# Kernel optimization log

Measured on AMD Instinct MI355X. Metric: run time of the kernel, lower is better.

Reference implementation:

```python
import jax, jax.numpy as jnp
import numpy as np

D_MODEL = 2048
N_HEADS = 32
N_KVHEADS = 8
HEAD_DIM = D_MODEL // N_HEADS  # 64
N_GROUPS = N_HEADS // N_KVHEADS  # 4
B, L = 2, 2048


def setup_inputs() -> dict:
    key = jax.random.key(0)
    k1, k2, k3 = jax.random.split(key, 3)
    x = jax.random.normal(k1, (B, L, D_MODEL), dtype=jnp.float32)
    W_qkv = jax.random.normal(k2, (D_MODEL, HEAD_DIM * (N_HEADS + 2 * N_KVHEADS)), dtype=jnp.float32) * 0.02
    W_out = jax.random.normal(k3, (D_MODEL, D_MODEL), dtype=jnp.float32) * 0.02
    # additive causal mask, broadcasts over (b, g, h, l, j)
    neg = jnp.float32(-1e9)
    mask = jnp.where(jnp.tril(jnp.ones((L, L), dtype=bool)), jnp.float32(0.0), neg)
    return {"x": x, "mask": mask, "W_qkv": W_qkv, "W_out": W_out}


def reference(x, mask, W_qkv, W_out):
    b, l, _ = x.shape
    qkv = x @ W_qkv  # (b, l, hd*(H + 2*KVH))
    q, k, v = jnp.split(qkv, [N_HEADS * HEAD_DIM, (N_HEADS + N_KVHEADS) * HEAD_DIM], axis=-1)
    # NOTE: faithful to the original: plain row-major reshapes (no seq/head transpose)
    q = q.reshape(b, N_GROUPS, N_KVHEADS, l, HEAD_DIM)  # (b, g, h, l, d)
    k = k.reshape(b, N_KVHEADS, l, HEAD_DIM)            # (b, h, j, d)
    v = v.reshape(b, N_KVHEADS, l, HEAD_DIM)            # (b, h, j, d)
    scores = jnp.einsum('bghld,bhjd->bghlj', q, k) * (HEAD_DIM ** -0.5)
    scores = scores + mask  # mask broadcasts over leading dims
    attn = jax.nn.softmax(scores, axis=-1)
    out = jnp.einsum('bghlj,bhjd->bghld', attn, v)  # (b, g, h, l, d)
    # rearrange 'b g h l d -> b l (g h d)'
    out = jnp.transpose(out, (0, 3, 1, 2, 4)).reshape(b, l, D_MODEL)
    return out @ W_out
```

## Files before the change

### kernel.cpp

```cpp
#include <hip/hip_runtime.h>
#include <stdint.h>


typedef unsigned short u16;
typedef unsigned int u32;
typedef __attribute__((ext_vector_type(8))) short bf16x8;
typedef __attribute__((ext_vector_type(4))) float f32x4;

__device__ __forceinline__ u16 f2bf(float f) {
  union { float f; uint32_t u; } v; v.f = f;
  uint32_t u = v.u;
  u += 0x7fffu + ((u >> 16) & 1u);
  return (u16)(u >> 16);
}

__device__ __forceinline__ f32x4 mfma16(bf16x8 a, bf16x8 b, f32x4 c) {
  return __builtin_amdgcn_mfma_f32_16x16x32_bf16(a, b, c, 0, 0, 0);
}

__device__ __forceinline__ uint32_t cvt_pk_bf16(float a, float b) {
  uint32_t r;
  asm("v_cvt_pk_bf16_f32 %0, %1, %2" : "=v"(r) : "v"(a), "v"(b));
  return r;
}

__device__ __forceinline__ float fmax3(float a, float b, float c) {
  float d;
  asm("v_max3_f32 %0, %1, %2, %3" : "=v"(d) : "v"(a), "v"(b), "v"(c));
  return d;
}

__device__ __forceinline__ float exp2fast(float x) {
  return __builtin_amdgcn_exp2f(x);
}

__device__ __forceinline__ void gload16(const u16* g, u16* l) {
  __builtin_amdgcn_global_load_lds((__attribute__((address_space(1))) void*)g,
                                   (__attribute__((address_space(3))) void*)l, 16, 0, 0);
}

__global__ __launch_bounds__(256) void cvt_f32_bf16(const float* __restrict__ in,
                                                    u16* __restrict__ out, int n4) {
  int i = blockIdx.x * blockDim.x + threadIdx.x;
  if (i < n4) {
    float4 v = ((const float4*)in)[i];
    uint2 o;
    o.x = (uint32_t)f2bf(v.x) | ((uint32_t)f2bf(v.y) << 16);
    o.y = (uint32_t)f2bf(v.z) | ((uint32_t)f2bf(v.w) << 16);
    ((uint2*)out)[i] = o;
  }
}

__global__ __launch_bounds__(256) void transpose_cvt(const float* __restrict__ in,
                                                     u16* __restrict__ out, int R, int C) {
  __shared__ float tile[32][33];
  int c0 = blockIdx.x * 32, r0 = blockIdx.y * 32;
  int tx = threadIdx.x, ty = threadIdx.y;
#pragma unroll
  for (int k = 0; k < 32; k += 8)
    tile[ty + k][tx] = in[(size_t)(r0 + ty + k) * C + c0 + tx];
  __syncthreads();
#pragma unroll
  for (int k = 0; k < 32; k += 8)
    out[(size_t)(c0 + ty + k) * R + r0 + tx] = f2bf(tile[tx][ty + k]);
}

template <bool OUTF32>
__global__ __launch_bounds__(256) void gemm_bf16(const u16* __restrict__ A,
                                                 const u16* __restrict__ Bt,
                                                 void* __restrict__ C,
                                                 int M, int N, int K) {
  __shared__ __align__(16) u16 As[2][128 * 32];
  __shared__ __align__(16) u16 Bs[2][128 * 32];
  int tid = threadIdx.x;
  int lane = tid & 63, w = tid >> 6;
  int wm = (w >> 1) * 64, wn = (w & 1) * 64;

  int nwg = gridDim.x * gridDim.y;
  int lin = blockIdx.y * gridDim.x + blockIdx.x;
  int lin2 = (lin & 7) * (nwg >> 3) + (lin >> 3);
  int bxs = lin2 % gridDim.x, bys = lin2 / gridDim.x;
  int bm = bys * 128, bn = bxs * 128;

  int c = lane & 15, g = lane >> 4;

  const int srow = w * 16 + (lane >> 2);
  const int scol = (((lane & 3) ^ ((lane >> 3) & 3))) * 8;
  const u16* aP = A + (size_t)(bm + srow) * K + scol;
  const u16* bP = Bt + (size_t)(bn + srow) * K + scol;
  const size_t rowskip = (size_t)64 * K;

  f32x4 zero = {0.f, 0.f, 0.f, 0.f};
  f32x4 acc[4][4];
#pragma unroll
  for (int mi = 0; mi < 4; mi++)
#pragma unroll
    for (int ni = 0; ni < 4; ni++) acc[mi][ni] = zero;

  auto STAGE = [&](int kt, int buf) {
    u16* aL = &As[buf][(w * 16) * 32];
    u16* bL = &Bs[buf][(w * 16) * 32];
    gload16(aP + kt, aL);
    gload16(aP + kt + rowskip, aL + 64 * 32);
    gload16(bP + kt, bL);
    gload16(bP + kt + rowskip, bL + 64 * 32);
  };

  const int nk = K >> 5;
  STAGE(0, 0);
  __syncthreads();

  const int fq = (g ^ ((c >> 1) & 3)) * 8;

  for (int t = 0; t < nk; ++t) {
    const int cur = t & 1;
    if (t + 1 < nk) STAGE((t + 1) << 5, cur ^ 1);
    bf16x8 af[4], bfr[4];
#pragma unroll
    for (int i = 0; i < 4; i++) af[i] = *(const bf16x8*)&As[cur][(wm + i * 16 + c) * 32 + fq];
#pragma unroll
    for (int i = 0; i < 4; i++) bfr[i] = *(const bf16x8*)&Bs[cur][(wn + i * 16 + c) * 32 + fq];
#pragma unroll
    for (int mi = 0; mi < 4; mi++)
#pragma unroll
      for (int ni = 0; ni < 4; ni++)
        acc[mi][ni] = mfma16(af[mi], bfr[ni], acc[mi][ni]);
    __syncthreads();
  }

#pragma unroll
  for (int mi = 0; mi < 4; mi++)
#pragma unroll
    for (int ni = 0; ni < 4; ni++)
#pragma unroll
      for (int i = 0; i < 4; i++) {
        int row = bm + wm + mi * 16 + g * 4 + i;
        int col = bn + wn + ni * 16 + c;
        float v = acc[mi][ni][i];
        if (OUTF32)
          ((float*)C)[(size_t)row * N + col] = v;
        else
          ((u16*)C)[(size_t)row * N + col] = f2bf(v);
      }
}

__global__ __launch_bounds__(256, 2) void attn_fwd(const u16* __restrict__ qkv,
                                                   u16* __restrict__ attn) {
  __shared__ __align__(16) u16 Ks[2][64][72];
  __shared__ __align__(16) u16 Vs[2][64][72];
  __shared__ __align__(16) u16 Ps[4][32][64];
  const int tid = threadIdx.x;
  const int lane = tid & 63, w = tid >> 6;
  const int c = lane & 15, g = lane >> 4;
  const float C2 = 0.18033688011112042f;

  const int bid = blockIdx.x;
  const int slot = bid >> 3;
  const int head = (bid & 7) * 8 + (slot >> 3);
  const int p = slot & 7;
  const int qtA = p, qtB = 15 - p;
  const int b = head >> 5, gh = head & 31, h = gh & 7;
  const u16* qb = qkv + (size_t)b * 6291456;
  const int qbaseA = qtA * 128 + w * 32;
  const int qbaseB = qtB * 128 + w * 32;

  const u16* qrowA = qb + (size_t)(gh * 64 + qtA * 4 + w) * 3072;
  const u16* qrowB = qb + (size_t)(gh * 64 + qtB * 4 + w) * 3072;
  bf16x8 qfA[2][2], qfB[2][2];
#pragma unroll
  for (int qs = 0; qs < 2; qs++)
#pragma unroll
    for (int kd = 0; kd < 2; kd++) {
      qfA[qs][kd] = *(const bf16x8*)(qrowA + (qs * 16 + c) * 64 + kd * 32 + g * 8);
      qfB[qs][kd] = *(const bf16x8*)(qrowB + (qs * 16 + c) * 64 + kd * 32 + g * 8);
    }

  const f32x4 zero = {0.f, 0.f, 0.f, 0.f};
  f32x4 oA[2][4], oB[2][4];
#pragma unroll
  for (int qs = 0; qs < 2; qs++)
#pragma unroll
    for (int dt = 0; dt < 4; dt++) { oA[qs][dt] = zero; oB[qs][dt] = zero; }
  float mA[2] = {-1e30f, -1e30f}, sA[2] = {0.f, 0.f};
  float mB[2] = {-1e30f, -1e30f}, sB[2] = {0.f, 0.f};

  const int kj = tid >> 2, kd16 = (tid & 3) * 16;
  const int vj0 = (tid >> 4) * 4, vd = (tid & 15) * 4;
  const int vsw = (tid & 7) << 3;
  uint4 kreg0, kreg1;
  uint2 vreg[4];

  auto LOAD = [&](int t) {
    int j = t * 64 + kj;
    const u16* kr = qb + (size_t)(h * 256 + (j >> 3)) * 3072 + 2048 + (j & 7) * 64;
    kreg0 = *(const uint4*)(kr + kd16);
    kreg1 = *(const uint4*)(kr + kd16 + 8);
#pragma unroll
    for (int r = 0; r < 4; r++) {
      int jv = t * 64 + vj0 + r;
      const u16* vr = qb + (size_t)(h * 256 + (jv >> 3)) * 3072 + 2560 + (jv & 7) * 64;
      vreg[r] = *(const uint2*)(vr + vd);
    }
  };
  auto EX = [](uint2 v, int e) -> uint32_t {
    uint32_t x = (e < 2) ? v.x : v.y;
    return (e & 1) ? (x >> 16) : (x & 0xffffu);
  };
  auto STORE = [&](int buf) {
    *(uint4*)&Ks[buf][kj][kd16] = kreg0;
    *(uint4*)&Ks[buf][kj][kd16 + 8] = kreg1;
#pragma unroll
    for (int e = 0; e < 4; e++) {
      uint2 wv;
      wv.x = EX(vreg[0], e) | (EX(vreg[1], e) << 16);
      wv.y = EX(vreg[2], e) | (EX(vreg[3], e) << 16);
      *(uint2*)&Vs[buf][vd + e][vj0 ^ vsw] = wv;
    }
  };

  auto computeQ = [&](int t, int qbase, bf16x8 (&qf)[2][2], bf16x8 (&kf)[4][2],
                      f32x4 (&o)[2][4], float (&m_i)[2], float (&s_i)[2], int cur) {
    const bool diag = (t * 64 + 63 > qbase);
#pragma unroll
    for (int qs = 0; qs < 2; qs++) {
      f32x4 sc[4];
      __builtin_amdgcn_s_setprio(1);
#pragma unroll
      for (int kvt = 0; kvt < 4; kvt++) {
        f32x4 s = mfma16(kf[kvt][0], qf[qs][0], zero);
        sc[kvt] = mfma16(kf[kvt][1], qf[qs][1], s);
      }
      __builtin_amdgcn_s_setprio(0);
      const int q = qbase + qs * 16 + c;
      if (diag) {
#pragma unroll
        for (int kvt = 0; kvt < 4; kvt++)
#pragma unroll
          for (int i = 0; i < 4; i++)
            if (t * 64 + kvt * 16 + g * 4 + i > q) sc[kvt][i] = -1e30f;
      }
      float tmax = fmax3(sc[0][0], sc[0][1], sc[0][2]);
      tmax = fmax3(tmax, sc[0][3], sc[1][0]);
      tmax = fmax3(tmax, sc[1][1], sc[1][2]);
      tmax = fmax3(tmax, sc[1][3], sc[2][0]);
      tmax = fmax3(tmax, sc[2][1], sc[2][2]);
      tmax = fmax3(tmax, sc[2][3], sc[3][0]);
      tmax = fmax3(tmax, sc[3][1], sc[3][2]);
      tmax = fmaxf(tmax, sc[3][3]);
      tmax = fmaxf(tmax, __shfl_xor(tmax, 16));
      tmax = fmaxf(tmax, __shfl_xor(tmax, 32));
      if (!__all(tmax <= m_i[qs] + 64.0f)) {
        float mn = fmaxf(m_i[qs], tmax);
        float corr = exp2fast((m_i[qs] - mn) * C2);
        m_i[qs] = mn;
        s_i[qs] *= corr;
#pragma unroll
        for (int i = 0; i < 4; i++) {
          float cb = __shfl(corr, g * 4 + i);
#pragma unroll
          for (int dt = 0; dt < 4; dt++) o[qs][dt][i] *= cb;
        }
      }
      const float nmc = -m_i[qs] * C2;
      float rs = 0.f;
#pragma unroll
      for (int kvt = 0; kvt < 4; kvt++)
#pragma unroll
        for (int i = 0; i < 4; i++) {
          float pv = exp2fast(fmaf(sc[kvt][i], C2, nmc));
          sc[kvt][i] = pv;
          rs += pv;
        }
      rs += __shfl_xor(rs, 16);
      rs += __shfl_xor(rs, 32);
      s_i[qs] += rs;
      const int pr = qs * 16 + c;
      const int sw = (c & 7) << 3;
#pragma unroll
      for (int kvt = 0; kvt < 4; kvt++) {
        uint2 pw;
        pw.x = cvt_pk_bf16(sc[kvt][0], sc[kvt][1]);
        pw.y = cvt_pk_bf16(sc[kvt][2], sc[kvt][3]);
        *(uint2*)&Ps[w][pr][(kvt * 16 + g * 4) ^ sw] = pw;
      }
    }
    __builtin_amdgcn_s_setprio(1);
#pragma unroll
    for (int kt2 = 0; kt2 < 2; kt2++) {
      bf16x8 bv[4];
#pragma unroll
      for (int dt = 0; dt < 4; dt++) {
        const int vr = dt * 16 + c;
        const int sv = ((dt * 4 + (c >> 2)) & 7) << 3;
        bv[dt] = *(const bf16x8*)&Vs[cur][vr][(kt2 * 32 + g * 8) ^ sv];
      }
#pragma unroll
      for (int qs = 0; qs < 2; qs++) {
        const int pr = qs * 16 + c;
        bf16x8 pa = *(const bf16x8*)&Ps[w][pr][(kt2 * 32 + g * 8) ^ ((c & 7) << 3)];
#pragma unroll
        for (int dt = 0; dt < 4; dt++) o[qs][dt] = mfma16(pa, bv[dt], o[qs][dt]);
      }
    }
    __builtin_amdgcn_s_setprio(0);
  };

  const int nt = 2 * qtB + 2;
  const int jtA = (qbaseA + 31) >> 6;
  const int jtB = (qbaseB + 31) >> 6;

  LOAD(0);
  STORE(0);
  __syncthreads();

  for (int t = 0; t < nt; ++t) {
    const int cur = t & 1;
    if (t + 1 < nt) LOAD(t + 1);
    if (t <= jtB) {
      bf16x8 kf[4][2];
#pragma unroll
      for (int kvt = 0; kvt < 4; kvt++)
#pragma unroll
        for (int kd = 0; kd < 2; kd++)
          kf[kvt][kd] = *(const bf16x8*)&Ks[cur][kvt * 16 + c][kd * 32 + g * 8];
      if (t <= jtA) computeQ(t, qbaseA, qfA, kf, oA, mA, sA, cur);
      computeQ(t, qbaseB, qfB, kf, oB, mB, sB, cur);
    }
    if (t + 1 < nt) STORE(cur ^ 1);
    __syncthreads();
  }

  auto epi = [&](int qbase, f32x4 (&o)[2][4], float (&s_i)[2]) {
#pragma unroll
    for (int qs = 0; qs < 2; qs++)
#pragma unroll
      for (int i = 0; i < 4; i++) {
        float sd = __shfl(s_i[qs], g * 4 + i);
        float inv = 1.0f / sd;
        int row = qbase + qs * 16 + g * 4 + i;
        u16* orow = attn + ((size_t)(b * 2048 + row)) * 2048 + gh * 64;
#pragma unroll
        for (int dt = 0; dt < 4; dt++) orow[dt * 16 + c] = f2bf(o[qs][dt][i] * inv);
      }
  };
  epi(qbaseA, oA, sA);
  epi(qbaseB, oB, sB);
}

extern "C" void kernel_launch(void* const* d_in, const int* in_sizes, int n_in,
                              void* d_out, int out_size, void* d_ws, size_t ws_size,
                              hipStream_t stream) {
  const float* x = (const float*)d_in[0];
  const float* Wqkv = (const float*)d_in[2];
  const float* Wout = (const float*)d_in[3];
  float* out = (float*)d_out;

  u16* xb = (u16*)d_ws;
  u16* wqkvT = xb + 8388608;
  u16* woutT = wqkvT + 6291456;
  u16* qkv = woutT + 4194304;
  u16* attn = qkv + 12582912;

  cvt_f32_bf16<<<8192, 256, 0, stream>>>(x, xb, 2097152);
  transpose_cvt<<<dim3(3072 / 32, 2048 / 32), dim3(32, 8), 0, stream>>>(Wqkv, wqkvT, 2048, 3072);
  transpose_cvt<<<dim3(2048 / 32, 2048 / 32), dim3(32, 8), 0, stream>>>(Wout, woutT, 2048, 2048);
  gemm_bf16<false><<<dim3(3072 / 128, 4096 / 128), 256, 0, stream>>>(xb, wqkvT, qkv, 4096, 3072, 2048);
  attn_fwd<<<512, 256, 0, stream>>>(qkv, attn);
  gemm_bf16<true><<<dim3(2048 / 128, 4096 / 128), 256, 0, stream>>>(attn, woutT, out, 4096, 2048, 2048);
}
```

Before: 195.8 us.

## Split attention work across 8 waves with 16 query rows each

The attention kernel now launches 512 threads per block (8 waves) instead of 256. Each wave handles 16 query rows per tile instead of 32, which halves the per-wave accumulator and register state so more waves can be resident. K and V shared-memory staging is redistributed across the larger thread count, and the K tile gains an XOR swizzle to cut LDS bank conflicts. The costs are more block-level synchronisation participants and redundant K fragment loads per wave.

Result: slower. 218.3 us (+11.5%).

```diff
diff --git a/kernel.cpp b/kernel.cpp
--- a/kernel.cpp
+++ b/kernel.cpp
@@ -144,11 +144,11 @@
       }
 }
 
-__global__ __launch_bounds__(256, 2) void attn_fwd(const u16* __restrict__ qkv,
+__global__ __launch_bounds__(512, 4) void attn_fwd(const u16* __restrict__ qkv,
                                                    u16* __restrict__ attn) {
   __shared__ __align__(16) u16 Ks[2][64][72];
   __shared__ __align__(16) u16 Vs[2][64][72];
-  __shared__ __align__(16) u16 Ps[4][32][64];
+  __shared__ __align__(16) u16 Ps[8][2][16][64];
   const int tid = threadIdx.x;
   const int lane = tid & 63, w = tid >> 6;
   const int c = lane & 15, g = lane >> 4;
@@ -161,153 +161,121 @@
   const int qtA = p, qtB = 15 - p;
   const int b = head >> 5, gh = head & 31, h = gh & 7;
   const u16* qb = qkv + (size_t)b * 6291456;
-  const int qbaseA = qtA * 128 + w * 32;
-  const int qbaseB = qtB * 128 + w * 32;
-
-  const u16* qrowA = qb + (size_t)(gh * 64 + qtA * 4 + w) * 3072;
-  const u16* qrowB = qb + (size_t)(gh * 64 + qtB * 4 + w) * 3072;
-  bf16x8 qfA[2][2], qfB[2][2];
-#pragma unroll
-  for (int qs = 0; qs < 2; qs++)
-#pragma unroll
-    for (int kd = 0; kd < 2; kd++) {
-      qfA[qs][kd] = *(const bf16x8*)(qrowA + (qs * 16 + c) * 64 + kd * 32 + g * 8);
-      qfB[qs][kd] = *(const bf16x8*)(qrowB + (qs * 16 + c) * 64 + kd * 32 + g * 8);
-    }
+  const int qbaseA = qtA * 128 + w * 16;
+  const int qbaseB = qtB * 128 + w * 16;
+
+  const u16* qpA = qb + (size_t)(gh * 64 + qtA * 4 + (w >> 1)) * 3072 + ((w & 1) * 16 + c) * 64;
+  const u16* qpB = qb + (size_t)(gh * 64 + qtB * 4 + (w >> 1)) * 3072 + ((w & 1) * 16 + c) * 64;
+  bf16x8 qfA[2], qfB[2];
+#pragma unroll
+  for (int kd = 0; kd < 2; kd++) {
+    qfA[kd] = *(const bf16x8*)(qpA + kd * 32 + g * 8);
+    qfB[kd] = *(const bf16x8*)(qpB + kd * 32 + g * 8);
+  }
 
   const f32x4 zero = {0.f, 0.f, 0.f, 0.f};
-  f32x4 oA[2][4], oB[2][4];
-#pragma unroll
-  for (int qs = 0; qs < 2; qs++)
-#pragma unroll
-    for (int dt = 0; dt < 4; dt++) { oA[qs][dt] = zero; oB[qs][dt] = zero; }
-  float mA[2] = {-1e30f, -1e30f}, sA[2] = {0.f, 0.f};
-  float mB[2] = {-1e30f, -1e30f}, sB[2] = {0.f, 0.f};
-
-  const int kj = tid >> 2, kd16 = (tid & 3) * 16;
-  const int vj0 = (tid >> 4) * 4, vd = (tid & 15) * 4;
-  const int vsw = (tid & 7) << 3;
-  uint4 kreg0, kreg1;
-  uint2 vreg[4];
+  f32x4 oA[4], oB[4];
+#pragma unroll
+  for (int dt = 0; dt < 4; dt++) { oA[dt] = zero; oB[dt] = zero; }
+  float mA = -1e30f, sA = 0.f, mB = -1e30f, sB = 0.f;
+
+  const int kj = tid >> 3, kd8 = (tid & 7) * 8;
+  const int ksw = (kj & 7) << 3;
+  const int vj0 = (tid & 31) * 2, vd = (tid >> 5) * 4;
+  uint4 kreg;
+  uint2 va, vb;
 
   auto LOAD = [&](int t) {
     int j = t * 64 + kj;
     const u16* kr = qb + (size_t)(h * 256 + (j >> 3)) * 3072 + 2048 + (j & 7) * 64;
-    kreg0 = *(const uint4*)(kr + kd16);
-    kreg1 = *(const uint4*)(kr + kd16 + 8);
-#pragma unroll
-    for (int r = 0; r < 4; r++) {
-      int jv = t * 64 + vj0 + r;
-      const u16* vr = qb + (size_t)(h * 256 + (jv >> 3)) * 3072 + 2560 + (jv & 7) * 64;
-      vreg[r] = *(const uint2*)(vr + vd);
-    }
+    kreg = *(const uint4*)(kr + kd8);
+    int jv0 = t * 64 + vj0;
+    const u16* vr0 = qb + (size_t)(h * 256 + (jv0 >> 3)) * 3072 + 2560 + (jv0 & 7) * 64;
+    int jv1 = jv0 + 1;
+    const u16* vr1 = qb + (size_t)(h * 256 + (jv1 >> 3)) * 3072 + 2560 + (jv1 & 7) * 64;
+    va = *(const uint2*)(vr0 + vd);
+    vb = *(const uint2*)(vr1 + vd);
   };
   auto EX = [](uint2 v, int e) -> uint32_t {
     uint32_t x = (e < 2) ? v.x : v.y;
     return (e & 1) ? (x >> 16) : (x & 0xffffu);
   };
   auto STORE = [&](int buf) {
-    *(uint4*)&Ks[buf][kj][kd16] = kreg0;
-    *(uint4*)&Ks[buf][kj][kd16 + 8] = kreg1;
+    *(uint4*)&Ks[buf][kj][kd8 ^ ksw] = kreg;
 #pragma unroll
     for (int e = 0; e < 4; e++) {
-      uint2 wv;
-      wv.x = EX(vreg[0], e) | (EX(vreg[1], e) << 16);
-      wv.y = EX(vreg[2], e) | (EX(vreg[3], e) << 16);
-      *(uint2*)&Vs[buf][vd + e][vj0 ^ vsw] = wv;
-    }
-  };
-
-  auto computeQ = [&](int t, int qbase, bf16x8 (&qf)[2][2], bf16x8 (&kf)[4][2],
-                      f32x4 (&o)[2][4], float (&m_i)[2], float (&s_i)[2], int cur) {
-    const bool diag = (t * 64 + 63 > qbase);
-#pragma unroll
-    for (int qs = 0; qs < 2; qs++) {
-      f32x4 sc[4];
-      __builtin_amdgcn_s_setprio(1);
-#pragma unroll
-      for (int kvt = 0; kvt < 4; kvt++) {
-        f32x4 s = mfma16(kf[kvt][0], qf[qs][0], zero);
-        sc[kvt] = mfma16(kf[kvt][1], qf[qs][1], s);
+      uint32_t wv = EX(va, e) | (EX(vb, e) << 16);
+      int d = vd + e;
+      *(u32*)&Vs[buf][d][vj0 ^ ((d & 7) << 3)] = wv;
+    }
+  };
+
+  auto scorePart = [&](int t, int qbase, bf16x8 (&qf)[2], bf16x8 (&kf)[4][2],
+                       float& m_i, float& s_i, f32x4 (&o)[4], int part) {
+    f32x4 sc[4];
+    __builtin_amdgcn_s_setprio(1);
+#pragma unroll
+    for (int kvt = 0; kvt < 4; kvt++) {
+      f32x4 s = mfma16(kf[kvt][0], qf[0], zero);
+      sc[kvt] = mfma16(kf[kvt][1], qf[1], s);
+    }
+    __builtin_amdgcn_s_setprio(0);
+    const int q = qbase + c;
+    if (t * 64 + 63 > qbase) {
+#pragma unroll
+      for (int kvt = 0; kvt < 4; kvt++)
+#pragma unroll
+        for (int i = 0; i < 4; i++)
+          if (t * 64 + kvt * 16 + g * 4 + i > q) sc[kvt][i] = -1e30f;
+    }
+    float tmax = fmax3(sc[0][0], sc[0][1], sc[0][2]);
+    tmax = fmax3(tmax, sc[0][3], sc[1][0]);
+    tmax = fmax3(tmax, sc[1][1], sc[1][2]);
+    tmax = fmax3(tmax, sc[1][3], sc[2][0]);
+    tmax = fmax3(tmax, sc[2][1], sc[2][2]);
+    tmax = fmax3(tmax, sc[2][3], sc[3][0]);
+    tmax = fmax3(tmax, sc[3][1], sc[3][2]);
+    tmax = fmaxf(tmax, sc[3][3]);
+    tmax = fmaxf(tmax, __shfl_xor(tmax, 16));
+    tmax = fmaxf(tmax, __shfl_xor(tmax, 32));
+    if (!__all(tmax <= m_i + 64.0f)) {
+      float mn = fmaxf(m_i, tmax);
+      float corr = exp2fast((m_i - mn) * C2);
+      m_i = mn;
+      s_i *= corr;
+#pragma unroll
+      for (int i = 0; i < 4; i++) {
+        float cb = __shfl(corr, g * 4 + i);
+#pragma unroll
+        for (int dt = 0; dt < 4; dt++) o[dt][i] *= cb;
       }
-      __builtin_amdgcn_s_setprio(0);
-      const int q = qbase + qs * 16 + c;
-      if (diag) {
-#pragma unroll
-        for (int kvt = 0; kvt < 4; kvt++)
-#pragma unroll
-          for (int i = 0; i < 4; i++)
-            if (t * 64 + kvt * 16 + g * 4 + i > q) sc[kvt][i] = -1e30f;
+    }
+    const float nmc = -m_i * C2;
+    float rs = 0.f;
+#pragma unroll
+    for (int kvt = 0; kvt < 4; kvt++)
+#pragma unroll
+      for (int i = 0; i < 4; i++) {
+        float pv = exp2fast(fmaf(sc[kvt][i], C2, nmc));
+        sc[kvt][i] = pv;
+        rs += pv;
       }
-      float tmax = fmax3(sc[0][0], sc[0][1], sc[0][2]);
-      tmax = fmax3(tmax, sc[0][3], sc[1][0]);
-      tmax = fmax3(tmax, sc[1][1], sc[1][2]);
-      tmax = fmax3(tmax, sc[1][3], sc[2][0]);
-      tmax = fmax3(tmax, sc[2][1], sc[2][2]);
-      tmax = fmax3(tmax, sc[2][3], sc[3][0]);
-      tmax = fmax3(tmax, sc[3][1], sc[3][2]);
-      tmax = fmaxf(tmax, sc[3][3]);
-      tmax = fmaxf(tmax, __shfl_xor(tmax, 16));
-      tmax = fmaxf(tmax, __shfl_xor(tmax, 32));
-      if (!__all(tmax <= m_i[qs] + 64.0f)) {
-        float mn = fmaxf(m_i[qs], tmax);
-        float corr = exp2fast((m_i[qs] - mn) * C2);
-        m_i[qs] = mn;
-        s_i[qs] *= corr;
-#pragma unroll
-        for (int i = 0; i < 4; i++) {
-          float cb = __shfl(corr, g * 4 + i);
-#pragma unroll
-          for (int dt = 0; dt < 4; dt++) o[qs][dt][i] *= cb;
-        }
-      }
-      const float nmc = -m_i[qs] * C2;
-      float rs = 0.f;
-#pragma unroll
-      for (int kvt = 0; kvt < 4; kvt++)
-#pragma unroll
-        for (int i = 0; i < 4; i++) {
-          float pv = exp2fast(fmaf(sc[kvt][i], C2, nmc));
-          sc[kvt][i] = pv;
-          rs += pv;
-        }
-      rs += __shfl_xor(rs, 16);
-      rs += __shfl_xor(rs, 32);
-      s_i[qs] += rs;
-      const int pr = qs * 16 + c;
-      const int sw = (c & 7) << 3;
-#pragma unroll
-      for (int kvt = 0; kvt < 4; kvt++) {
-        uint2 pw;
-        pw.x = cvt_pk_bf16(sc[kvt][0], sc[kvt][1]);
-        pw.y = cvt_pk_bf16(sc[kvt][2], sc[kvt][3]);
-        *(uint2*)&Ps[w][pr][(kvt * 16 + g * 4) ^ sw] = pw;
-      }
-    }
-    __builtin_amdgcn_s_setprio(1);
-#pragma unroll
-    for (int kt2 = 0; kt2 < 2; kt2++) {
-      bf16x8 bv[4];
-#pragma unroll
-      for (int dt = 0; dt < 4; dt++) {
-        const int vr = dt * 16 + c;
-        const int sv = ((dt * 4 + (c >> 2)) & 7) << 3;
-        bv[dt] = *(const bf16x8*)&Vs[cur][vr][(kt2 * 32 + g * 8) ^ sv];
-      }
-#pragma unroll
-      for (int qs = 0; qs < 2; qs++) {
-        const int pr = qs * 16 + c;
-        bf16x8 pa = *(const bf16x8*)&Ps[w][pr][(kt2 * 32 + g * 8) ^ ((c & 7) << 3)];
-#pragma unroll
-        for (int dt = 0; dt < 4; dt++) o[qs][dt] = mfma16(pa, bv[dt], o[qs][dt]);
-      }
-    }
-    __builtin_amdgcn_s_setprio(0);
+    rs += __shfl_xor(rs, 16);
+    rs += __shfl_xor(rs, 32);
+    s_i += rs;
+    const int sw = (c & 7) << 3;
+#pragma unroll
+    for (int kvt = 0; kvt < 4; kvt++) {
+      uint2 pw;
+      pw.x = cvt_pk_bf16(sc[kvt][0], sc[kvt][1]);
+      pw.y = cvt_pk_bf16(sc[kvt][2], sc[kvt][3]);
+      *(uint2*)&Ps[w][part][c][(kvt * 16 + g * 4) ^ sw] = pw;
+    }
   };
 
   const int nt = 2 * qtB + 2;
-  const int jtA = (qbaseA + 31) >> 6;
-  const int jtB = (qbaseB + 31) >> 6;
+  const int jtA = (qbaseA + 15) >> 6;
+  const int jtB = (qbaseB + 15) >> 6;
 
   LOAD(0);
   STORE(0);
@@ -317,31 +285,50 @@
     const int cur = t & 1;
     if (t + 1 < nt) LOAD(t + 1);
     if (t <= jtB) {
+      const int sw = (c & 7) << 3;
       bf16x8 kf[4][2];
 #pragma unroll
       for (int kvt = 0; kvt < 4; kvt++)
 #pragma unroll
         for (int kd = 0; kd < 2; kd++)
-          kf[kvt][kd] = *(const bf16x8*)&Ks[cur][kvt * 16 + c][kd * 32 + g * 8];
-      if (t <= jtA) computeQ(t, qbaseA, qfA, kf, oA, mA, sA, cur);
-      computeQ(t, qbaseB, qfB, kf, oB, mB, sB, cur);
+          kf[kvt][kd] = *(const bf16x8*)&Ks[cur][kvt * 16 + c][(kd * 32 + g * 8) ^ sw];
+      const bool doA = (t <= jtA);
+      if (doA) scorePart(t, qbaseA, qfA, kf, mA, sA, oA, 0);
+      scorePart(t, qbaseB, qfB, kf, mB, sB, oB, 1);
+      __builtin_amdgcn_s_setprio(1);
+#pragma unroll
+      for (int kt2 = 0; kt2 < 2; kt2++) {
+        bf16x8 bv[4];
+#pragma unroll
+        for (int dt = 0; dt < 4; dt++)
+          bv[dt] = *(const bf16x8*)&Vs[cur][dt * 16 + c][(kt2 * 32 + g * 8) ^ sw];
+        if (doA) {
+          bf16x8 pa = *(const bf16x8*)&Ps[w][0][c][(kt2 * 32 + g * 8) ^ sw];
+#pragma unroll
+          for (int dt = 0; dt < 4; dt++) oA[dt] = mfma16(pa, bv[dt], oA[dt]);
+        }
+        {
+          bf16x8 pb = *(const bf16x8*)&Ps[w][1][c][(kt2 * 32 + g * 8) ^ sw];
+#pragma unroll
+          for (int dt = 0; dt < 4; dt++) oB[dt] = mfma16(pb, bv[dt], oB[dt]);
+        }
+      }
+      __builtin_amdgcn_s_setprio(0);
     }
     if (t + 1 < nt) STORE(cur ^ 1);
     __syncthreads();
   }
 
-  auto epi = [&](int qbase, f32x4 (&o)[2][4], float (&s_i)[2]) {
-#pragma unroll
-    for (int qs = 0; qs < 2; qs++)
-#pragma unroll
-      for (int i = 0; i < 4; i++) {
-        float sd = __shfl(s_i[qs], g * 4 + i);
-        float inv = 1.0f / sd;
-        int row = qbase + qs * 16 + g * 4 + i;
-        u16* orow = attn + ((size_t)(b * 2048 + row)) * 2048 + gh * 64;
-#pragma unroll
-        for (int dt = 0; dt < 4; dt++) orow[dt * 16 + c] = f2bf(o[qs][dt][i] * inv);
-      }
+  auto epi = [&](int qbase, f32x4 (&o)[4], float s_i) {
+#pragma unroll
+    for (int i = 0; i < 4; i++) {
+      float sd = __shfl(s_i, g * 4 + i);
+      float inv = 1.0f / sd;
+      int row = qbase + g * 4 + i;
+      u16* orow = attn + ((size_t)(b * 2048 + row)) * 2048 + gh * 64;
+#pragma unroll
+      for (int dt = 0; dt < 4; dt++) orow[dt * 16 + c] = f2bf(o[dt][i] * inv);
+    }
   };
   epi(qbaseA, oA, sA);
   epi(qbaseB, oB, sB);
@@ -365,6 +352,6 @@
   transpose_cvt<<<dim3(3072 / 32, 2048 / 32), dim3(32, 8), 0, stream>>>(Wqkv, wqkvT, 2048, 3072);
   transpose_cvt<<<dim3(2048 / 32, 2048 / 32), dim3(32, 8), 0, stream>>>(Wout, woutT, 2048, 2048);
   gemm_bf16<false><<<dim3(3072 / 128, 4096 / 128), 256, 0, stream>>>(xb, wqkvT, qkv, 4096, 3072, 2048);
-  attn_fwd<<<512, 256, 0, stream>>>(qkv, attn);
+  attn_fwd<<<512, 512, 0, stream>>>(qkv, attn);
   gemm_bf16<true><<<dim3(2048 / 128, 4096 / 128), 256, 0, stream>>>(attn, woutT, out, 4096, 2048, 2048);
 }
```
